# Optimization experiments

Measured on AMD Instinct MI355X. Metric: run time of the kernel, lower is better.

The kernel has to match this reference:

```python
import jax, jax.numpy as jnp
import numpy as np

B, N, C = 2, 8192, 256
H = 8
CH = C // H  # head dim 32
M = 32       # nbhd size
HID = 512    # mlp hidden = 2.0 * dim
TAB = 3025   # pre_table rows (55x55 relative positions)
POSF = 5     # pos_dim + 3


def _ln(x, w, b):
    mu = jnp.mean(x, axis=-1, keepdims=True)
    var = jnp.var(x, axis=-1, keepdims=True)
    return (x - mu) / jnp.sqrt(var + 1e-5) * w + b


def setup_inputs() -> dict:
    key = jax.random.key(0)
    ks = jax.random.split(key, 24)
    s = lambda fan: 1.0 / np.sqrt(fan)
    inp = {
        'feat': jax.random.normal(ks[0], (B, N, C), jnp.float32),
        'member_idx': jax.random.randint(ks[1], (B, N, M), 0, N),
        'cluster_mask': jnp.ones((B, N, M), jnp.float32),
        'pe_idx': jax.random.randint(ks[2], (B, N, M), 0, TAB),
        'global_attn': 0,
        'pre_table': jax.random.normal(ks[3], (TAB, POSF), jnp.float32),
        'norm1_w': jnp.ones((C,), jnp.float32),
        'norm1_b': jnp.zeros((C,), jnp.float32),
        'q_w': jax.random.normal(ks[4], (C, C), jnp.float32) * s(C),
        'q_b': jnp.zeros((C,), jnp.float32),
        'kv_w': jax.random.normal(ks[5], (2 * C, C), jnp.float32) * s(C),
        'kv_b': jnp.zeros((2 * C,), jnp.float32),
        'blank_k': jax.random.normal(ks[6], (C,), jnp.float32),
        'blank_v': jax.random.normal(ks[7], (C,), jnp.float32),
        'pe_w': jax.random.normal(ks[8], (H, POSF), jnp.float32) * s(POSF),
        'pe_b': jnp.zeros((H,), jnp.float32),
        'proj_w': jax.random.normal(ks[9], (C, C), jnp.float32) * s(C),
        'proj_b': jnp.zeros((C,), jnp.float32),
        'norm2_w': jnp.ones((C,), jnp.float32),
        'norm2_b': jnp.zeros((C,), jnp.float32),
        'fc1_w': jax.random.normal(ks[10], (HID, C), jnp.float32) * s(C),
        'fc1_b': jnp.zeros((HID,), jnp.float32),
        'fc2_w': jax.random.normal(ks[11], (C, HID), jnp.float32) * s(HID),
        'fc2_b': jnp.zeros((C,), jnp.float32),
    }
    return inp


def _block(feat, member_idx, cluster_mask, pe_idx, pre_table,
           norm1_w, norm1_b, q_w, q_b, kv_w, kv_b, blank_k, blank_v,
           pe_w, pe_b, proj_w, proj_b, norm2_w, norm2_b,
           fc1_w, fc1_b, fc2_w, fc2_b):
    b, n, c = feat.shape
    h, c_ = H, c // H
    scale = c_ ** -0.5
    shortcut = feat
    x = _ln(feat, norm1_w, norm1_b)
    q = (x @ q_w.T + q_b) * scale                     # b n c
    kv = (x @ kv_w.T + kv_b).reshape(b, n, h, 2, c_)  # torch view layout
    k = kv[..., 0, :]                                 # b n h c_
    v = kv[..., 1, :]
    q = q.reshape(b, n, h, c_)
    bidx = jnp.arange(b)[:, None, None]
    k_g = k[bidx, member_idx]                         # b n m h c_ (gather)
    attn = jnp.einsum('bnhc,bnmhc->bhnm', q, k_g)     # CLUSTENQK
    pe_table = pre_table @ pe_w.T + pe_b              # TAB h
    pos = pe_table[pe_idx]                            # b n m h
    attn = attn + pos.transpose(0, 3, 1, 2)
    attn = attn + (1.0 - cluster_mask)[:, None, :, :] * (-100.0)
    blank = jnp.einsum('bnhc,hc->bhn', q, blank_k.reshape(h, c_))
    blank = jnp.clip(blank, -5.0, 5.0)[..., None]     # b h n 1
    attn = jnp.concatenate([attn, blank], axis=-1)
    attn = jax.nn.softmax(attn, axis=-1)
    blank_a = attn[..., -1:]
    attn = attn[..., :-1]
    v_g = v[bidx, member_idx]                         # b n m h c_
    out = jnp.einsum('bhnm,bnmhc->bnhc', attn, v_g)   # CLUSTENAV
    out = out + blank_a.transpose(0, 2, 1, 3) * blank_v.reshape(1, 1, h, c_)
    out = out.reshape(b, n, c)
    out = out @ proj_w.T + proj_b
    x = shortcut + out
    y = _ln(x, norm2_w, norm2_b)
    y = jax.nn.gelu(y @ fc1_w.T + fc1_b, approximate=False)
    y = y @ fc2_w.T + fc2_b
    return x + y


def reference(feat, member_idx, cluster_mask, pe_idx, global_attn, pre_table,
              norm1_w, norm1_b, q_w, q_b, kv_w, kv_b, blank_k, blank_v,
              pe_w, pe_b, proj_w, proj_b, norm2_w, norm2_b,
              fc1_w, fc1_b, fc2_w, fc2_b):
    # global_attn is False (local cluster attention path)
    return _block(feat, member_idx, cluster_mask, pe_idx, pre_table,
                  norm1_w, norm1_b, q_w, q_b, kv_w, kv_b, blank_k, blank_v,
                  pe_w, pe_b, proj_w, proj_b, norm2_w, norm2_b,
                  fc1_w, fc1_b, fc2_w, fc2_b)
```

## Files before the change

### kernel.cpp

```cpp
#include <hip/hip_runtime.h>
#include <math.h>

namespace {
constexpr int kN    = 8192;
constexpr int kC    = 256;
constexpr int kTAB  = 3025;
constexpr int kRowsTotal = 2 * kN;
constexpr float kScale = 0.17677669529663687f;
}

typedef __attribute__((ext_vector_type(8))) short bf16x8;
typedef __attribute__((ext_vector_type(4))) float f32x4;
typedef _Float16 h8 __attribute__((ext_vector_type(8)));
typedef _Float16 h4 __attribute__((ext_vector_type(4)));

__device__ __forceinline__ unsigned short f2bf(float f) {
  unsigned int u = __float_as_uint(f);
  u += 0x7fffu + ((u >> 16) & 1u);
  return (unsigned short)(u >> 16);
}
__device__ __forceinline__ float bflo(unsigned int u) {
  return __uint_as_float(u << 16);
}
__device__ __forceinline__ float bfhi(unsigned int u) {
  return __uint_as_float(u & 0xffff0000u);
}
__device__ __forceinline__ unsigned short f2h(float f) {
  _Float16 h = (_Float16)f;
  unsigned short u;
  __builtin_memcpy(&u, &h, 2);
  return u;
}
__device__ __forceinline__ float h2f(unsigned short u) {
  _Float16 h;
  __builtin_memcpy(&h, &u, 2);
  return (float)h;
}

#define GLOAD16(g, l)                                                   \
  __builtin_amdgcn_global_load_lds(                                     \
      (const __attribute__((address_space(1))) void*)(g),               \
      (__attribute__((address_space(3))) void*)(l), 16, 0, 0)

__global__ __launch_bounds__(256) void ln_bf16_kernel(
    const float* __restrict__ x, const float* __restrict__ w,
    const float* __restrict__ b, unsigned short* __restrict__ o) {
  int t = threadIdx.x;
  int row = blockIdx.x * 4 + (t >> 6);
  int l = t & 63;
  float4 v = *(const float4*)(x + (size_t)row * kC + l * 4);
  float s  = v.x + v.y + v.z + v.w;
  float s2 = v.x * v.x + v.y * v.y + v.z * v.z + v.w * v.w;
#pragma unroll
  for (int d = 1; d < 64; d <<= 1) {
    s  += __shfl_xor(s, d, 64);
    s2 += __shfl_xor(s2, d, 64);
  }
  float mu = s * (1.0f / kC);
  float rstd = rsqrtf(s2 * (1.0f / kC) - mu * mu + 1e-5f);
  float4 wv = *(const float4*)(w + l * 4);
  float4 bv = *(const float4*)(b + l * 4);
  unsigned short o0 = f2bf((v.x - mu) * rstd * wv.x + bv.x);
  unsigned short o1 = f2bf((v.y - mu) * rstd * wv.y + bv.y);
  unsigned short o2 = f2bf((v.z - mu) * rstd * wv.z + bv.z);
  unsigned short o3 = f2bf((v.w - mu) * rstd * wv.w + bv.w);
  uint2 ov;
  ov.x = ((unsigned int)o1 << 16) | o0;
  ov.y = ((unsigned int)o3 << 16) | o2;
  *(uint2*)(o + (size_t)row * kC + l * 4) = ov;
}

__global__ __launch_bounds__(256) void pe_kernel(const float* __restrict__ tab,
                                                 const float* __restrict__ pw,
                                                 const float* __restrict__ pb,
                                                 float* __restrict__ outp) {
  int i = blockIdx.x * 256 + threadIdx.x;
  if (i >= kTAB * 8) return;
  int r = i >> 3, h = i & 7;
  float acc = pb[h];
#pragma unroll
  for (int f = 0; f < 5; ++f) acc += tab[r * 5 + f] * pw[h * 5 + f];
  outp[i] = acc;
}

__global__ __launch_bounds__(256) void pos_precompute_kernel(
    const int* __restrict__ pe_idx, const float* __restrict__ pe_full,
    const float* __restrict__ cmask, unsigned short* __restrict__ posm) {
  int i = blockIdx.x * 256 + threadIdx.x;
  int row = i >> 8, m = (i >> 3) & 31, h = i & 7;
  int idx = pe_idx[(size_t)row * 32 + m];
  float v = pe_full[(size_t)idx * 8 + h] +
            (1.0f - cmask[(size_t)row * 32 + m]) * -100.0f;
  posm[(size_t)row * 256 + h * 32 + m] = f2h(v);
}

__global__ __launch_bounds__(256) void cast_weights_kernel(
    const float* __restrict__ qw, const float* __restrict__ kvw,
    const float* __restrict__ pjw, const float* __restrict__ f1w,
    const float* __restrict__ f2w, const float* __restrict__ qb,
    const float* __restrict__ kvb, const float* __restrict__ bk,
    unsigned short* __restrict__ wqkv, unsigned short* __restrict__ wproj,
    unsigned short* __restrict__ wfc1, unsigned short* __restrict__ wfc2,
    float* __restrict__ bqkv, unsigned short* __restrict__ bkh) {
  int i = blockIdx.x * 256 + threadIdx.x;
  if (i < 65536)       wqkv[i]            = f2bf(qw[i]);
  else if (i < 196608) wqkv[i]            = f2bf(kvw[i - 65536]);
  else if (i < 262144) wproj[i - 196608]  = f2bf(pjw[i - 196608]);
  else if (i < 393216) wfc1[i - 262144]   = f2bf(f1w[i - 262144]);
  else if (i < 524288) wfc2[i - 393216]   = f2bf(f2w[i - 393216]);
  else if (i < 524544) bqkv[i - 524288]   = qb[i - 524288];
  else if (i < 525056) bqkv[i - 524288]   = kvb[i - 524544];
  else if (i < 525312) bkh[i - 525056]    = f2h(bk[i - 525056]);
}

template <int EPI, int KDIM>
__global__ __launch_bounds__(512) void gemm64(
    const unsigned short* __restrict__ A, const unsigned short* __restrict__ Wt,
    const float* __restrict__ bias, void* __restrict__ o1,
    unsigned short* __restrict__ o2, unsigned short* __restrict__ o3,
    const float* __restrict__ res, const float* __restrict__ w2,
    const float* __restrict__ b2, unsigned short* __restrict__ yln) {
  __shared__ alignas(16) unsigned short smem[40960];
  unsigned short* As0 = smem;
  unsigned short* Bs0 = smem + 8192;
  int t = threadIdx.x;
  int w = t >> 6, l = t & 63;
  int bm = blockIdx.x * 64, bn = blockIdx.y * 256;

  f32x4 acc[4][2] = {};

  const size_t aoff = (size_t)(bm + w * 8 + (l >> 3)) * KDIM + (l & 7) * 8;
  const size_t boff = (size_t)(bn + w * 32 + (l >> 3)) * KDIM + (l & 7) * 8;
  const int lr = l & 15, lk = l >> 4;

#define STAGE_T(buf, k0)                                                      \
  do {                                                                        \
    GLOAD16(A + aoff + (k0), As0 + (buf)*4096 + w * 512 + l * 8);             \
    GLOAD16(Wt + boff + (k0), Bs0 + (buf)*16384 + w * 2048 + l * 8);          \
    GLOAD16(Wt + boff + (k0) + (size_t)8 * KDIM,                              \
            Bs0 + (buf)*16384 + w * 2048 + 512 + l * 8);                      \
    GLOAD16(Wt + boff + (k0) + (size_t)16 * KDIM,                             \
            Bs0 + (buf)*16384 + w * 2048 + 1024 + l * 8);                     \
    GLOAD16(Wt + boff + (k0) + (size_t)24 * KDIM,                             \
            Bs0 + (buf)*16384 + w * 2048 + 1536 + l * 8);                     \
  } while (0)

  auto compute = [&](int buf) {
#pragma unroll
    for (int kk = 0; kk < 2; ++kk) {
      bf16x8 af[4], bfr[2];
#pragma unroll
      for (int mi = 0; mi < 4; ++mi)
        af[mi] = *(const bf16x8*)(As0 + buf * 4096 + (mi * 16 + lr) * 64 +
                                  kk * 32 + lk * 8);
#pragma unroll
      for (int ni = 0; ni < 2; ++ni)
        bfr[ni] = *(const bf16x8*)(Bs0 + buf * 16384 +
                                   (w * 32 + ni * 16 + lr) * 64 + kk * 32 +
                                   lk * 8);
#pragma unroll
      for (int mi = 0; mi < 4; ++mi)
#pragma unroll
        for (int ni = 0; ni < 2; ++ni)
          acc[mi][ni] = __builtin_amdgcn_mfma_f32_16x16x32_bf16(
              af[mi], bfr[ni], acc[mi][ni], 0, 0, 0);
    }
  };

  STAGE_T(0, 0);
  __syncthreads();
  int cur = 0;
#pragma unroll
  for (int k0 = 64; k0 < KDIM; k0 += 64) {
    STAGE_T(cur ^ 1, k0);
    compute(cur);
    __syncthreads();
    cur ^= 1;
  }
  compute(cur);

  if constexpr (EPI == 1) {
    __syncthreads();
    float* xs = (float*)smem;
#pragma unroll
    for (int mi = 0; mi < 4; ++mi) {
#pragma unroll
      for (int ni = 0; ni < 2; ++ni) {
        int c = w * 32 + ni * 16 + lr;
        float bv = bias[c];
#pragma unroll
        for (int j = 0; j < 4; ++j) {
          int rl = mi * 16 + lk * 4 + j;
          float x = acc[mi][ni][j] + bv + res[(size_t)(bm + rl) * 256 + c];
          xs[rl * 260 + c] = x;
          ((float*)o1)[(size_t)(bm + rl) * 256 + c] = x;
        }
      }
    }
    __syncthreads();
    int r = t >> 3, sub = t & 7;
    float4 xv[8];
    float sx = 0.f, sxx = 0.f;
#pragma unroll
    for (int i = 0; i < 8; ++i) {
      xv[i] = *(const float4*)&xs[r * 260 + sub * 4 + i * 32];
      sx  += xv[i].x + xv[i].y + xv[i].z + xv[i].w;
      sxx += xv[i].x * xv[i].x + xv[i].y * xv[i].y + xv[i].z * xv[i].z +
             xv[i].w * xv[i].w;
    }
#pragma unroll
    for (int d = 1; d < 8; d <<= 1) {
      sx  += __shfl_xor(sx, d, 64);
      sxx += __shfl_xor(sxx, d, 64);
    }
    float mu = sx * (1.0f / 256.0f);
    float rstd = rsqrtf(sxx * (1.0f / 256.0f) - mu * mu + 1e-5f);
#pragma unroll
    for (int i = 0; i < 8; ++i) {
      int c = sub * 4 + i * 32;
      float4 wv = *(const float4*)(w2 + c);
      float4 bv = *(const float4*)(b2 + c);
      unsigned short y0 = f2bf((xv[i].x - mu) * rstd * wv.x + bv.x);
      unsigned short y1 = f2bf((xv[i].y - mu) * rstd * wv.y + bv.y);
      unsigned short y2 = f2bf((xv[i].z - mu) * rstd * wv.z + bv.z);
      unsigned short y3 = f2bf((xv[i].w - mu) * rstd * wv.w + bv.w);
      uint2 ov;
      ov.x = ((unsigned int)y1 << 16) | y0;
      ov.y = ((unsigned int)y3 << 16) | y2;
      *(uint2*)(yln + (size_t)(bm + r) * 256 + c) = ov;
    }
  } else {
#pragma unroll
    for (int mi = 0; mi < 4; ++mi) {
#pragma unroll
      for (int ni = 0; ni < 2; ++ni) {
        int col = bn + w * 32 + ni * 16 + lr;
        float bv = bias[col];
#pragma unroll
        for (int j = 0; j < 4; ++j) {
          int rg = bm + mi * 16 + lk * 4 + j;
          float x = acc[mi][ni][j] + bv;
          if constexpr (EPI == 0) {
            if (col < 256) {
              ((unsigned short*)o1)[(size_t)rg * 256 + col] = f2h(x * kScale);
            } else {
              int c = col - 256;
              int h = c >> 6, sbit = (c >> 5) & 1, ch = c & 31;
              unsigned short* dst = sbit ? o3 : o2;
              dst[(size_t)rg * 256 + h * 32 + ch] = f2h(x);
            }
          } else if constexpr (EPI == 2) {
            float g = 0.5f * x * (1.0f + erff(x * 0.70710678118654752f));
            ((unsigned short*)o1)[(size_t)rg * 512 + col] = f2bf(g);
          } else {
            ((float*)o1)[(size_t)rg * 256 + col] =
                res[(size_t)rg * 256 + col] + x;
          }
        }
      }
    }
  }
#undef STAGE_T
}

__global__ __launch_bounds__(256) void attn_kernel(
    const unsigned short* __restrict__ q, const unsigned short* __restrict__ k,
    const unsigned short* __restrict__ v, const int* __restrict__ member_idx,
    const unsigned short* __restrict__ posm,
    const unsigned short* __restrict__ bkh, const float* __restrict__ blank_v,
    unsigned short* __restrict__ outp) {
  int t = threadIdx.x;
  int w = t >> 6, l = t & 63;
  int bid = blockIdx.x;
  int part = bid & 7;
  int bb = part >> 2, hg = part & 3;
  int row = bb * kN + (bid >> 3) * 4 + w;
  const unsigned int kvbyte = (unsigned int)bb * (kN * 512u);

  __shared__ float        aw[4][2][36];
  __shared__ unsigned int offs[4][32];
  __shared__ float        posl[4][2][32];

  {
    int m = l & 31, hloc = l >> 5;
    posl[w][hloc][m] = h2f(posm[(size_t)row * 256 + hg * 64 + l]);
    if (l < 32)
      offs[w][l] =
          kvbyte + (unsigned int)member_idx[(size_t)row * 32 + l] * 512u;
  }
  __syncthreads();

  const int m8 = l >> 3, ch = l & 7;
  const int hsel = ch >> 2;

  h8 qv8 = *(const h8*)(q + (size_t)row * 256 + hg * 64 + ch * 8);

  float lg[4];
#pragma unroll
  for (int i = 0; i < 4; ++i) {
    int mi = i * 8 + m8;
    const char* kp = (const char*)k + offs[w][mi] + hg * 128 + ch * 16;
    h8 kv = *(const h8*)kp;
    float p = 0.f;
#pragma unroll
    for (int e = 0; e < 8; ++e) p = fmaf((float)qv8[e], (float)kv[e], p);
    p += __shfl_xor(p, 1, 64);
    p += __shfl_xor(p, 2, 64);
    lg[i] = p + posl[w][hsel][mi];
  }

  float bl = 0.f;
  {
    h8 bk8 = *(const h8*)(bkh + hg * 64 + ch * 8);
#pragma unroll
    for (int e = 0; e < 8; ++e) bl = fmaf((float)qv8[e], (float)bk8[e], bl);
    bl += __shfl_xor(bl, 1, 64);
    bl += __shfl_xor(bl, 2, 64);
    bl = fminf(fmaxf(bl, -5.0f), 5.0f);
  }

  float mx = fmaxf(fmaxf(lg[0], lg[1]), fmaxf(lg[2], lg[3]));
  mx = fmaxf(mx, __shfl_xor(mx, 8, 64));
  mx = fmaxf(mx, __shfl_xor(mx, 16, 64));
  mx = fmaxf(mx, __shfl_xor(mx, 32, 64));
  mx = fmaxf(mx, bl);
  float e4[4], s = 0.f;
#pragma unroll
  for (int i = 0; i < 4; ++i) { e4[i] = __expf(lg[i] - mx); s += e4[i]; }
  s += __shfl_xor(s, 8, 64);
  s += __shfl_xor(s, 16, 64);
  s += __shfl_xor(s, 32, 64);
  float eb = __expf(bl - mx);
  s += eb;
  float inv = __builtin_amdgcn_rcpf(s);
  if ((ch & 3) == 0) {
#pragma unroll
    for (int i = 0; i < 4; ++i) aw[w][hsel][i * 8 + m8] = e4[i] * inv;
    if (m8 == 0) aw[w][hsel][32] = eb * inv;
  }
  __syncthreads();

  const int hp = l >> 5, sq = (l >> 3) & 3, c8 = l & 7;
  const char* vb = (const char*)v + (hg * 2 + hp) * 64 + c8 * 8;
  float a0 = 0.f, a1 = 0.f, a2 = 0.f, a3 = 0.f;
#pragma unroll
  for (int i = 0; i < 8; ++i) {
    int mm = sq * 8 + i;
    float a = aw[w][hp][mm];
    h4 u = *(const h4*)(vb + offs[w][mm]);
    a0 = fmaf(a, (float)u[0], a0);
    a1 = fmaf(a, (float)u[1], a1);
    a2 = fmaf(a, (float)u[2], a2);
    a3 = fmaf(a, (float)u[3], a3);
  }
  a0 += __shfl_xor(a0, 8, 64);  a1 += __shfl_xor(a1, 8, 64);
  a2 += __shfl_xor(a2, 8, 64);  a3 += __shfl_xor(a3, 8, 64);
  a0 += __shfl_xor(a0, 16, 64); a1 += __shfl_xor(a1, 16, 64);
  a2 += __shfl_xor(a2, 16, 64); a3 += __shfl_xor(a3, 16, 64);
  if (sq == 0) {
    float ab = aw[w][hp][32];
    int c = (hg * 2 + hp) * 32 + c8 * 4;
    float4 bv = *(const float4*)(blank_v + c);
    a0 = fmaf(ab, bv.x, a0);
    a1 = fmaf(ab, bv.y, a1);
    a2 = fmaf(ab, bv.z, a2);
    a3 = fmaf(ab, bv.w, a3);
    uint2 o;
    o.x = ((unsigned int)f2bf(a1) << 16) | f2bf(a0);
    o.y = ((unsigned int)f2bf(a3) << 16) | f2bf(a2);
    *(uint2*)(outp + (size_t)row * 256 + c) = o;
  }
}

extern "C" void kernel_launch(void* const* d_in, const int* in_sizes, int n_in,
                              void* d_out, int out_size, void* d_ws, size_t ws_size,
                              hipStream_t stream) {
  const float* feat       = (const float*)d_in[0];
  const int*   member_idx = (const int*)d_in[1];
  const float* cmask      = (const float*)d_in[2];
  const int*   pe_idx     = (const int*)d_in[3];
  const float* pre_table  = (const float*)d_in[5];
  const float* n1w        = (const float*)d_in[6];
  const float* n1b        = (const float*)d_in[7];
  const float* q_w        = (const float*)d_in[8];
  const float* q_b        = (const float*)d_in[9];
  const float* kv_w       = (const float*)d_in[10];
  const float* kv_b       = (const float*)d_in[11];
  const float* blank_k    = (const float*)d_in[12];
  const float* blank_v    = (const float*)d_in[13];
  const float* pe_w       = (const float*)d_in[14];
  const float* pe_b       = (const float*)d_in[15];
  const float* proj_w     = (const float*)d_in[16];
  const float* proj_b     = (const float*)d_in[17];
  const float* n2w        = (const float*)d_in[18];
  const float* n2b        = (const float*)d_in[19];
  const float* fc1_w      = (const float*)d_in[20];
  const float* fc1_b      = (const float*)d_in[21];
  const float* fc2_w      = (const float*)d_in[22];
  const float* fc2_b      = (const float*)d_in[23];

  float* out = (float*)d_out;
  unsigned char* ws = (unsigned char*)d_ws;

  unsigned short* xln   = (unsigned short*)(ws + 0);
  unsigned short* q_buf = (unsigned short*)(ws + 8388608);
  unsigned short* k_buf = (unsigned short*)(ws + 16777216);
  unsigned short* v_buf = (unsigned short*)(ws + 25165824);
  unsigned short* wqkv  = (unsigned short*)(ws + 33554432);
  unsigned short* wproj = (unsigned short*)(ws + 33947648);
  unsigned short* wfc1  = (unsigned short*)(ws + 34078720);
  unsigned short* wfc2  = (unsigned short*)(ws + 34340864);
  float*          bqkv  = (float*)(ws + 34603008);
  float*          pe_buf= (float*)(ws + 34606080);
  unsigned short* bkh   = (unsigned short*)(ws + 34704000);
  unsigned short* attn_out = xln;
  unsigned short* yln   = q_buf;
  unsigned short* h1    = k_buf;
  unsigned short* posm  = (unsigned short*)out;

  cast_weights_kernel<<<2052, 256, 0, stream>>>(
      q_w, kv_w, proj_w, fc1_w, fc2_w, q_b, kv_b, blank_k, wqkv, wproj, wfc1,
      wfc2, bqkv, bkh);
  pe_kernel<<<(kTAB * 8 + 255) / 256, 256, 0, stream>>>(pre_table, pe_w, pe_b, pe_buf);
  ln_bf16_kernel<<<kRowsTotal / 4, 256, 0, stream>>>(feat, n1w, n1b, xln);
  pos_precompute_kernel<<<kRowsTotal, 256, 0, stream>>>(pe_idx, pe_buf, cmask, posm);

  gemm64<0, 256><<<dim3(kRowsTotal / 64, 3), 512, 0, stream>>>(
      xln, wqkv, bqkv, q_buf, k_buf, v_buf, nullptr, nullptr, nullptr, nullptr);

  attn_kernel<<<kRowsTotal, 256, 0, stream>>>(
      q_buf, k_buf, v_buf, member_idx, posm, bkh, blank_v, attn_out);

  gemm64<1, 256><<<dim3(kRowsTotal / 64, 1), 512, 0, stream>>>(
      attn_out, wproj, proj_b, out, nullptr, nullptr, feat, n2w, n2b, yln);

  gemm64<2, 256><<<dim3(kRowsTotal / 64, 2), 512, 0, stream>>>(
      yln, wfc1, fc1_b, h1, nullptr, nullptr, nullptr, nullptr, nullptr, nullptr);

  gemm64<3, 512><<<dim3(kRowsTotal / 64, 1), 512, 0, stream>>>(
      h1, wfc2, fc2_b, out, nullptr, nullptr, out, nullptr, nullptr, nullptr);
}
```

Baseline: 124.2 us.

## Fuse proj, LN2, fc1+GELU and fc2 into one MLP kernel; merge prep kernels

Replaces the separate projection, fc1 and fc2 GEMM launches with one per-64-row-tile kernel. The residual, LN2 output and GELU hidden activations stay in LDS and registers instead of round-tripping through global memory. The four preprocessing kernels (weight cast, pe table, LN1, pos precompute) are merged into one launch, and the pe projection is now computed inline per element. The cost is a large LDS footprint (about 130KB), only 256 blocks of 512 threads, and serialized fc1 and fc2 per tile, which may lower occupancy and parallelism.

```diff
diff --git a/kernel.cpp b/kernel.cpp
--- a/kernel.cpp
+++ b/kernel.cpp
@@ -4,7 +4,6 @@
 namespace {
 constexpr int kN    = 8192;
 constexpr int kC    = 256;
-constexpr int kTAB  = 3025;
 constexpr int kRowsTotal = 2 * kN;
 constexpr float kScale = 0.17677669529663687f;
 }
@@ -42,84 +41,70 @@
       (const __attribute__((address_space(1))) void*)(g),               \
       (__attribute__((address_space(3))) void*)(l), 16, 0, 0)
 
-__global__ __launch_bounds__(256) void ln_bf16_kernel(
-    const float* __restrict__ x, const float* __restrict__ w,
-    const float* __restrict__ b, unsigned short* __restrict__ o) {
-  int t = threadIdx.x;
-  int row = blockIdx.x * 4 + (t >> 6);
-  int l = t & 63;
-  float4 v = *(const float4*)(x + (size_t)row * kC + l * 4);
-  float s  = v.x + v.y + v.z + v.w;
-  float s2 = v.x * v.x + v.y * v.y + v.z * v.z + v.w * v.w;
-#pragma unroll
-  for (int d = 1; d < 64; d <<= 1) {
-    s  += __shfl_xor(s, d, 64);
-    s2 += __shfl_xor(s2, d, 64);
-  }
-  float mu = s * (1.0f / kC);
-  float rstd = rsqrtf(s2 * (1.0f / kC) - mu * mu + 1e-5f);
-  float4 wv = *(const float4*)(w + l * 4);
-  float4 bv = *(const float4*)(b + l * 4);
-  unsigned short o0 = f2bf((v.x - mu) * rstd * wv.x + bv.x);
-  unsigned short o1 = f2bf((v.y - mu) * rstd * wv.y + bv.y);
-  unsigned short o2 = f2bf((v.z - mu) * rstd * wv.z + bv.z);
-  unsigned short o3 = f2bf((v.w - mu) * rstd * wv.w + bv.w);
-  uint2 ov;
-  ov.x = ((unsigned int)o1 << 16) | o0;
-  ov.y = ((unsigned int)o3 << 16) | o2;
-  *(uint2*)(o + (size_t)row * kC + l * 4) = ov;
-}
-
-__global__ __launch_bounds__(256) void pe_kernel(const float* __restrict__ tab,
-                                                 const float* __restrict__ pw,
-                                                 const float* __restrict__ pb,
-                                                 float* __restrict__ outp) {
-  int i = blockIdx.x * 256 + threadIdx.x;
-  if (i >= kTAB * 8) return;
-  int r = i >> 3, h = i & 7;
-  float acc = pb[h];
-#pragma unroll
-  for (int f = 0; f < 5; ++f) acc += tab[r * 5 + f] * pw[h * 5 + f];
-  outp[i] = acc;
-}
-
-__global__ __launch_bounds__(256) void pos_precompute_kernel(
-    const int* __restrict__ pe_idx, const float* __restrict__ pe_full,
-    const float* __restrict__ cmask, unsigned short* __restrict__ posm) {
-  int i = blockIdx.x * 256 + threadIdx.x;
-  int row = i >> 8, m = (i >> 3) & 31, h = i & 7;
-  int idx = pe_idx[(size_t)row * 32 + m];
-  float v = pe_full[(size_t)idx * 8 + h] +
-            (1.0f - cmask[(size_t)row * 32 + m]) * -100.0f;
-  posm[(size_t)row * 256 + h * 32 + m] = f2h(v);
-}
-
-__global__ __launch_bounds__(256) void cast_weights_kernel(
+__global__ __launch_bounds__(256) void prep_kernel(
     const float* __restrict__ qw, const float* __restrict__ kvw,
     const float* __restrict__ pjw, const float* __restrict__ f1w,
     const float* __restrict__ f2w, const float* __restrict__ qb,
     const float* __restrict__ kvb, const float* __restrict__ bk,
+    const float* __restrict__ feat, const float* __restrict__ n1w,
+    const float* __restrict__ n1b, const int* __restrict__ pe_idx,
+    const float* __restrict__ pre_table, const float* __restrict__ pe_w,
+    const float* __restrict__ pe_b, const float* __restrict__ cmask,
     unsigned short* __restrict__ wqkv, unsigned short* __restrict__ wproj,
     unsigned short* __restrict__ wfc1, unsigned short* __restrict__ wfc2,
-    float* __restrict__ bqkv, unsigned short* __restrict__ bkh) {
-  int i = blockIdx.x * 256 + threadIdx.x;
-  if (i < 65536)       wqkv[i]            = f2bf(qw[i]);
-  else if (i < 196608) wqkv[i]            = f2bf(kvw[i - 65536]);
-  else if (i < 262144) wproj[i - 196608]  = f2bf(pjw[i - 196608]);
-  else if (i < 393216) wfc1[i - 262144]   = f2bf(f1w[i - 262144]);
-  else if (i < 524288) wfc2[i - 393216]   = f2bf(f2w[i - 393216]);
-  else if (i < 524544) bqkv[i - 524288]   = qb[i - 524288];
-  else if (i < 525056) bqkv[i - 524288]   = kvb[i - 524544];
-  else if (i < 525312) bkh[i - 525056]    = f2h(bk[i - 525056]);
+    float* __restrict__ bqkv, unsigned short* __restrict__ bkh,
+    unsigned short* __restrict__ xln, unsigned short* __restrict__ posm) {
+  int bid = blockIdx.x;
+  int t = threadIdx.x;
+  if (bid < 2052) {
+    int i = bid * 256 + t;
+    if (i < 65536)       wqkv[i]            = f2bf(qw[i]);
+    else if (i < 196608) wqkv[i]            = f2bf(kvw[i - 65536]);
+    else if (i < 262144) wproj[i - 196608]  = f2bf(pjw[i - 196608]);
+    else if (i < 393216) wfc1[i - 262144]   = f2bf(f1w[i - 262144]);
+    else if (i < 524288) wfc2[i - 393216]   = f2bf(f2w[i - 393216]);
+    else if (i < 524544) bqkv[i - 524288]   = qb[i - 524288];
+    else if (i < 525056) bqkv[i - 524288]   = kvb[i - 524544];
+    else if (i < 525312) bkh[i - 525056]    = f2h(bk[i - 525056]);
+  } else if (bid < 6148) {
+    int row = (bid - 2052) * 4 + (t >> 6);
+    int l = t & 63;
+    float4 v = *(const float4*)(feat + (size_t)row * kC + l * 4);
+    float s  = v.x + v.y + v.z + v.w;
+    float s2 = v.x * v.x + v.y * v.y + v.z * v.z + v.w * v.w;
+#pragma unroll
+    for (int d = 1; d < 64; d <<= 1) {
+      s  += __shfl_xor(s, d, 64);
+      s2 += __shfl_xor(s2, d, 64);
+    }
+    float mu = s * (1.0f / kC);
+    float rstd = rsqrtf(s2 * (1.0f / kC) - mu * mu + 1e-5f);
+    float4 wv = *(const float4*)(n1w + l * 4);
+    float4 bv = *(const float4*)(n1b + l * 4);
+    uint2 ov;
+    ov.x = ((unsigned int)f2bf((v.y - mu) * rstd * wv.y + bv.y) << 16) |
+           f2bf((v.x - mu) * rstd * wv.x + bv.x);
+    ov.y = ((unsigned int)f2bf((v.w - mu) * rstd * wv.w + bv.w) << 16) |
+           f2bf((v.z - mu) * rstd * wv.z + bv.z);
+    *(uint2*)(xln + (size_t)row * kC + l * 4) = ov;
+  } else {
+    int i = (bid - 6148) * 256 + t;
+    int row = i >> 8, m = (i >> 3) & 31, h = i & 7;
+    int idx = pe_idx[(size_t)row * 32 + m];
+    float acc = pe_b[h];
+#pragma unroll
+    for (int f = 0; f < 5; ++f)
+      acc += pre_table[idx * 5 + f] * pe_w[h * 5 + f];
+    acc += (1.0f - cmask[(size_t)row * 32 + m]) * -100.0f;
+    posm[(size_t)row * 256 + h * 32 + m] = f2h(acc);
+  }
 }
 
 template <int EPI, int KDIM>
 __global__ __launch_bounds__(512) void gemm64(
     const unsigned short* __restrict__ A, const unsigned short* __restrict__ Wt,
     const float* __restrict__ bias, void* __restrict__ o1,
-    unsigned short* __restrict__ o2, unsigned short* __restrict__ o3,
-    const float* __restrict__ res, const float* __restrict__ w2,
-    const float* __restrict__ b2, unsigned short* __restrict__ yln) {
+    unsigned short* __restrict__ o2, unsigned short* __restrict__ o3) {
   __shared__ alignas(16) unsigned short smem[40960];
   unsigned short* As0 = smem;
   unsigned short* Bs0 = smem + 8192;
@@ -179,25 +164,116 @@
   }
   compute(cur);
 
-  if constexpr (EPI == 1) {
-    __syncthreads();
-    float* xs = (float*)smem;
-#pragma unroll
-    for (int mi = 0; mi < 4; ++mi) {
-#pragma unroll
-      for (int ni = 0; ni < 2; ++ni) {
-        int c = w * 32 + ni * 16 + lr;
-        float bv = bias[c];
-#pragma unroll
-        for (int j = 0; j < 4; ++j) {
-          int rl = mi * 16 + lk * 4 + j;
-          float x = acc[mi][ni][j] + bv + res[(size_t)(bm + rl) * 256 + c];
-          xs[rl * 260 + c] = x;
-          ((float*)o1)[(size_t)(bm + rl) * 256 + c] = x;
+#pragma unroll
+  for (int mi = 0; mi < 4; ++mi) {
+#pragma unroll
+    for (int ni = 0; ni < 2; ++ni) {
+      int col = bn + w * 32 + ni * 16 + lr;
+      float bv = bias[col];
+#pragma unroll
+      for (int j = 0; j < 4; ++j) {
+        int rg = bm + mi * 16 + lk * 4 + j;
+        float x = acc[mi][ni][j] + bv;
+        if (col < 256) {
+          ((unsigned short*)o1)[(size_t)rg * 256 + col] = f2h(x * kScale);
+        } else {
+          int c = col - 256;
+          int h = c >> 6, sbit = (c >> 5) & 1, ch = c & 31;
+          unsigned short* dst = sbit ? o3 : o2;
+          dst[(size_t)rg * 256 + h * 32 + ch] = f2h(x);
         }
       }
     }
+  }
+#undef STAGE_T
+}
+
+__global__ __launch_bounds__(512) void mlp_fused(
+    const unsigned short* __restrict__ A,
+    const unsigned short* __restrict__ Wp,
+    const float* __restrict__ pbias,
+    const float* __restrict__ feat,
+    const float* __restrict__ w2, const float* __restrict__ b2,
+    const unsigned short* __restrict__ W1, const float* __restrict__ b1,
+    const unsigned short* __restrict__ W2, const float* __restrict__ b2f,
+    float* __restrict__ outp) {
+  __shared__ alignas(16) unsigned short sm[66560];
+  int t = threadIdx.x;
+  int w = t >> 6, l = t & 63;
+  int bm = blockIdx.x * 64;
+  const int lr = l & 15, lk = l >> 4;
+
+  f32x4 accp[4][2] = {};
+  {
+    const size_t aoff = (size_t)(bm + w * 8 + (l >> 3)) * 256 + (l & 7) * 8;
+    const size_t boff = (size_t)(w * 32 + (l >> 3)) * 256 + (l & 7) * 8;
+#define PSTAGE(buf, k0)                                                       \
+  do {                                                                        \
+    GLOAD16(A + aoff + (k0), sm + (buf)*4096 + w * 512 + l * 8);              \
+    GLOAD16(Wp + boff + (k0), sm + 8192 + (buf)*16384 + w * 2048 + l * 8);    \
+    GLOAD16(Wp + boff + (k0) + (size_t)2048,                                  \
+            sm + 8192 + (buf)*16384 + w * 2048 + 512 + l * 8);                \
+    GLOAD16(Wp + boff + (k0) + (size_t)4096,                                  \
+            sm + 8192 + (buf)*16384 + w * 2048 + 1024 + l * 8);               \
+    GLOAD16(Wp + boff + (k0) + (size_t)6144,                                  \
+            sm + 8192 + (buf)*16384 + w * 2048 + 1536 + l * 8);               \
+  } while (0)
+    auto computeP = [&](int buf) {
+#pragma unroll
+      for (int kk = 0; kk < 2; ++kk) {
+        bf16x8 af[4], bfr[2];
+#pragma unroll
+        for (int mi = 0; mi < 4; ++mi)
+          af[mi] = *(const bf16x8*)(sm + buf * 4096 + (mi * 16 + lr) * 64 +
+                                    kk * 32 + lk * 8);
+#pragma unroll
+        for (int ni = 0; ni < 2; ++ni)
+          bfr[ni] = *(const bf16x8*)(sm + 8192 + buf * 16384 +
+                                     (w * 32 + ni * 16 + lr) * 64 + kk * 32 +
+                                     lk * 8);
+#pragma unroll
+        for (int mi = 0; mi < 4; ++mi)
+#pragma unroll
+          for (int ni = 0; ni < 2; ++ni)
+            accp[mi][ni] = __builtin_amdgcn_mfma_f32_16x16x32_bf16(
+                af[mi], bfr[ni], accp[mi][ni], 0, 0, 0);
+      }
+    };
+    PSTAGE(0, 0);
     __syncthreads();
+    int cur = 0;
+#pragma unroll
+    for (int k0 = 64; k0 < 256; k0 += 64) {
+      PSTAGE(cur ^ 1, k0);
+      computeP(cur);
+      __syncthreads();
+      cur ^= 1;
+    }
+    computeP(cur);
+#undef PSTAGE
+  }
+
+  f32x4 xr[4][2];
+  float* xs = (float*)sm;
+  __syncthreads();
+#pragma unroll
+  for (int mi = 0; mi < 4; ++mi) {
+#pragma unroll
+    for (int ni = 0; ni < 2; ++ni) {
+      int c = w * 32 + ni * 16 + lr;
+      float bv = pbias[c];
+#pragma unroll
+      for (int j = 0; j < 4; ++j) {
+        int rl = mi * 16 + lk * 4 + j;
+        float x = accp[mi][ni][j] + bv + feat[(size_t)(bm + rl) * 256 + c];
+        xr[mi][ni][j] = x;
+        xs[rl * 260 + c] = x;
+      }
+    }
+  }
+  __syncthreads();
+
+  {
     int r = t >> 3, sub = t & 7;
     float4 xv[8];
     float sx = 0.f, sxx = 0.f;
@@ -220,47 +296,137 @@
       int c = sub * 4 + i * 32;
       float4 wv = *(const float4*)(w2 + c);
       float4 bv = *(const float4*)(b2 + c);
-      unsigned short y0 = f2bf((xv[i].x - mu) * rstd * wv.x + bv.x);
-      unsigned short y1 = f2bf((xv[i].y - mu) * rstd * wv.y + bv.y);
-      unsigned short y2 = f2bf((xv[i].z - mu) * rstd * wv.z + bv.z);
-      unsigned short y3 = f2bf((xv[i].w - mu) * rstd * wv.w + bv.w);
       uint2 ov;
-      ov.x = ((unsigned int)y1 << 16) | y0;
-      ov.y = ((unsigned int)y3 << 16) | y2;
-      *(uint2*)(yln + (size_t)(bm + r) * 256 + c) = ov;
-    }
-  } else {
+      ov.x = ((unsigned int)f2bf((xv[i].y - mu) * rstd * wv.y + bv.y) << 16) |
+             f2bf((xv[i].x - mu) * rstd * wv.x + bv.x);
+      ov.y = ((unsigned int)f2bf((xv[i].w - mu) * rstd * wv.w + bv.w) << 16) |
+             f2bf((xv[i].z - mu) * rstd * wv.z + bv.z);
+      *(uint2*)&sm[49664 + r * 264 + c] = ov;
+    }
+  }
+  __syncthreads();
+
+  const int FB = 33280;
+#define F1STAGE(buf, k0, c)                                                   \
+  do {                                                                        \
+    GLOAD16(W1 + (size_t)((c)*256 + w * 32 + (l >> 2)) * 256 + (k0) +         \
+                (l & 3) * 8,                                                  \
+            sm + FB + (buf)*8192 + w * 1024 + l * 8);                         \
+    GLOAD16(W1 + (size_t)((c)*256 + w * 32 + 16 + (l >> 2)) * 256 + (k0) +    \
+                (l & 3) * 8,                                                  \
+            sm + FB + (buf)*8192 + w * 1024 + 512 + l * 8);                   \
+  } while (0)
+#pragma unroll
+  for (int c = 0; c < 2; ++c) {
+    f32x4 accf[4][2] = {};
+    auto computeF1 = [&](int buf, int ka) {
+      bf16x8 af[4], bfr[2];
+#pragma unroll
+      for (int mi = 0; mi < 4; ++mi)
+        af[mi] =
+            *(const bf16x8*)(sm + 49664 + (mi * 16 + lr) * 264 + ka + lk * 8);
+#pragma unroll
+      for (int ni = 0; ni < 2; ++ni)
+        bfr[ni] = *(const bf16x8*)(sm + FB + buf * 8192 +
+                                   (w * 32 + ni * 16 + lr) * 32 + lk * 8);
+#pragma unroll
+      for (int mi = 0; mi < 4; ++mi)
+#pragma unroll
+        for (int ni = 0; ni < 2; ++ni)
+          accf[mi][ni] = __builtin_amdgcn_mfma_f32_16x16x32_bf16(
+              af[mi], bfr[ni], accf[mi][ni], 0, 0, 0);
+    };
+    F1STAGE(0, 0, c);
+    __syncthreads();
+    int cur = 0;
+#pragma unroll
+    for (int k0 = 32; k0 < 256; k0 += 32) {
+      F1STAGE(cur ^ 1, k0, c);
+      computeF1(cur, k0 - 32);
+      __syncthreads();
+      cur ^= 1;
+    }
+    computeF1(cur, 224);
+    __syncthreads();
 #pragma unroll
     for (int mi = 0; mi < 4; ++mi) {
 #pragma unroll
       for (int ni = 0; ni < 2; ++ni) {
-        int col = bn + w * 32 + ni * 16 + lr;
-        float bv = bias[col];
+        int colg = c * 256 + w * 32 + ni * 16 + lr;
+        float bv = b1[colg];
 #pragma unroll
         for (int j = 0; j < 4; ++j) {
-          int rg = bm + mi * 16 + lk * 4 + j;
-          float x = acc[mi][ni][j] + bv;
-          if constexpr (EPI == 0) {
-            if (col < 256) {
-              ((unsigned short*)o1)[(size_t)rg * 256 + col] = f2h(x * kScale);
-            } else {
-              int c = col - 256;
-              int h = c >> 6, sbit = (c >> 5) & 1, ch = c & 31;
-              unsigned short* dst = sbit ? o3 : o2;
-              dst[(size_t)rg * 256 + h * 32 + ch] = f2h(x);
-            }
-          } else if constexpr (EPI == 2) {
-            float g = 0.5f * x * (1.0f + erff(x * 0.70710678118654752f));
-            ((unsigned short*)o1)[(size_t)rg * 512 + col] = f2bf(g);
-          } else {
-            ((float*)o1)[(size_t)rg * 256 + col] =
-                res[(size_t)rg * 256 + col] + x;
-          }
+          float x = accf[mi][ni][j] + bv;
+          float g = 0.5f * x * (1.0f + erff(x * 0.70710678118654752f));
+          sm[(mi * 16 + lk * 4 + j) * 520 + colg] = f2bf(g);
         }
       }
     }
   }
-#undef STAGE_T
+#undef F1STAGE
+  __syncthreads();
+
+  f32x4 acc2[4][2] = {};
+#define F2STAGE(buf, k0)                                                      \
+  do {                                                                        \
+    GLOAD16(W2 + (size_t)(w * 32 + (l >> 3)) * 512 + (k0) + (l & 7) * 8,      \
+            sm + FB + (buf)*16384 + w * 2048 + l * 8);                        \
+    GLOAD16(W2 + (size_t)(w * 32 + 8 + (l >> 3)) * 512 + (k0) + (l & 7) * 8,  \
+            sm + FB + (buf)*16384 + w * 2048 + 512 + l * 8);                  \
+    GLOAD16(W2 + (size_t)(w * 32 + 16 + (l >> 3)) * 512 + (k0) + (l & 7) * 8, \
+            sm + FB + (buf)*16384 + w * 2048 + 1024 + l * 8);                 \
+    GLOAD16(W2 + (size_t)(w * 32 + 24 + (l >> 3)) * 512 + (k0) + (l & 7) * 8, \
+            sm + FB + (buf)*16384 + w * 2048 + 1536 + l * 8);                 \
+  } while (0)
+  {
+    auto computeF2 = [&](int buf, int ka) {
+#pragma unroll
+      for (int kk = 0; kk < 2; ++kk) {
+        bf16x8 af[4], bfr[2];
+#pragma unroll
+        for (int mi = 0; mi < 4; ++mi)
+          af[mi] = *(const bf16x8*)(sm + (mi * 16 + lr) * 520 + ka + kk * 32 +
+                                    lk * 8);
+#pragma unroll
+        for (int ni = 0; ni < 2; ++ni)
+          bfr[ni] = *(const bf16x8*)(sm + FB + buf * 16384 +
+                                     (w * 32 + ni * 16 + lr) * 64 + kk * 32 +
+                                     lk * 8);
+#pragma unroll
+        for (int mi = 0; mi < 4; ++mi)
+#pragma unroll
+          for (int ni = 0; ni < 2; ++ni)
+            acc2[mi][ni] = __builtin_amdgcn_mfma_f32_16x16x32_bf16(
+                af[mi], bfr[ni], acc2[mi][ni], 0, 0, 0);
+      }
+    };
+    F2STAGE(0, 0);
+    __syncthreads();
+    int cur = 0;
+#pragma unroll
+    for (int k0 = 64; k0 < 512; k0 += 64) {
+      F2STAGE(cur ^ 1, k0);
+      computeF2(cur, k0 - 64);
+      __syncthreads();
+      cur ^= 1;
+    }
+    computeF2(cur, 448);
+  }
+#undef F2STAGE
+
+#pragma unroll
+  for (int mi = 0; mi < 4; ++mi) {
+#pragma unroll
+    for (int ni = 0; ni < 2; ++ni) {
+      int col = w * 32 + ni * 16 + lr;
+      float bv = b2f[col];
+#pragma unroll
+      for (int j = 0; j < 4; ++j) {
+        int rg = bm + mi * 16 + lk * 4 + j;
+        outp[(size_t)rg * 256 + col] = xr[mi][ni][j] + acc2[mi][ni][j] + bv;
+      }
+    }
+  }
 }
 
 __global__ __launch_bounds__(256) void attn_kernel(
@@ -411,32 +577,21 @@
   unsigned short* wfc1  = (unsigned short*)(ws + 34078720);
   unsigned short* wfc2  = (unsigned short*)(ws + 34340864);
   float*          bqkv  = (float*)(ws + 34603008);
-  float*          pe_buf= (float*)(ws + 34606080);
-  unsigned short* bkh   = (unsigned short*)(ws + 34704000);
+  unsigned short* bkh   = (unsigned short*)(ws + 34606080);
   unsigned short* attn_out = xln;
-  unsigned short* yln   = q_buf;
-  unsigned short* h1    = k_buf;
   unsigned short* posm  = (unsigned short*)out;
 
-  cast_weights_kernel<<<2052, 256, 0, stream>>>(
-      q_w, kv_w, proj_w, fc1_w, fc2_w, q_b, kv_b, blank_k, wqkv, wproj, wfc1,
-      wfc2, bqkv, bkh);
-  pe_kernel<<<(kTAB * 8 + 255) / 256, 256, 0, stream>>>(pre_table, pe_w, pe_b, pe_buf);
-  ln_bf16_kernel<<<kRowsTotal / 4, 256, 0, stream>>>(feat, n1w, n1b, xln);
-  pos_precompute_kernel<<<kRowsTotal, 256, 0, stream>>>(pe_idx, pe_buf, cmask, posm);
+  prep_kernel<<<22532, 256, 0, stream>>>(
+      q_w, kv_w, proj_w, fc1_w, fc2_w, q_b, kv_b, blank_k, feat, n1w, n1b,
+      pe_idx, pre_table, pe_w, pe_b, cmask, wqkv, wproj, wfc1, wfc2, bqkv,
+      bkh, xln, posm);
 
   gemm64<0, 256><<<dim3(kRowsTotal / 64, 3), 512, 0, stream>>>(
-      xln, wqkv, bqkv, q_buf, k_buf, v_buf, nullptr, nullptr, nullptr, nullptr);
+      xln, wqkv, bqkv, q_buf, k_buf, v_buf);
 
   attn_kernel<<<kRowsTotal, 256, 0, stream>>>(
       q_buf, k_buf, v_buf, member_idx, posm, bkh, blank_v, attn_out);
 
-  gemm64<1, 256><<<dim3(kRowsTotal / 64, 1), 512, 0, stream>>>(
-      attn_out, wproj, proj_b, out, nullptr, nullptr, feat, n2w, n2b, yln);
-
-  gemm64<2, 256><<<dim3(kRowsTotal / 64, 2), 512, 0, stream>>>(
-      yln, wfc1, fc1_b, h1, nullptr, nullptr, nullptr, nullptr, nullptr, nullptr);
-
-  gemm64<3, 512><<<dim3(kRowsTotal / 64, 1), 512, 0, stream>>>(
-      h1, wfc2, fc2_b, out, nullptr, nullptr, out, nullptr, nullptr, nullptr);
-}
+  mlp_fused<<<kRowsTotal / 64, 512, 0, stream>>>(
+      attn_out, wproj, proj_b, feat, n2w, n2b, wfc1, fc1_b, wfc2, fc2_b, out);
+}
```

After: 108.7 us. -12.5%, faster.
